# Optimization experiments

Measured on AMD Instinct MI355X. Metric: run time of the kernel, lower is better.

The kernel has to match this reference:

```python
import jax, jax.numpy as jnp
import numpy as np

EMBED_DIM = 1024
NUM_HEADS = 16
HEAD_DIM = EMBED_DIM // NUM_HEADS


def setup_inputs() -> dict:
    key = jax.random.key(0)
    ks = jax.random.split(key, 9)
    B, S, E = 4, 2048, EMBED_DIM
    # xavier_uniform bound for square [E, E] weights
    bound = float(np.sqrt(6.0 / (E + E)))
    def w(k):
        return jax.random.uniform(k, (E, E), jnp.float32, -bound, bound)
    return {
        "x": jax.random.normal(ks[0], (B, S, E), jnp.float32),
        "Wq": w(ks[1]), "bq": jnp.zeros((E,), jnp.float32),
        "Wk": w(ks[2]), "bk": jnp.zeros((E,), jnp.float32),
        "Wv": w(ks[3]), "bv": jnp.zeros((E,), jnp.float32),
        "Wo": w(ks[4]), "bo": jnp.zeros((E,), jnp.float32),
    }


def reference(x, Wq, bq, Wk, bk, Wv, bv, Wo, bo):
    B, S, E = x.shape
    H, D = NUM_HEADS, HEAD_DIM
    # Linear projections (torch Linear: x @ W.T + b)
    q = (x @ Wq.T + bq).reshape(B, S, H, D)
    k = (x @ Wk.T + bk).reshape(B, S, H, D)
    v = (x @ Wv.T + bv).reshape(B, S, H, D)
    # per-head scaled dot-product attention (vectorized over heads)
    scores = jnp.einsum("bqhd,bkhd->bhqk", q, k) / jnp.sqrt(jnp.float32(D))
    attn = jax.nn.softmax(scores, axis=-1)
    o = jnp.einsum("bhqk,bkhd->bqhd", attn, v).reshape(B, S, E)
    return o @ Wo.T + bo
```

## Files before the change

kernel.cpp:

```cpp
#include <hip/hip_runtime.h>
#include <stdint.h>

typedef unsigned short u16;
typedef short bf16x8 __attribute__((ext_vector_type(8)));
typedef float f32x4 __attribute__((ext_vector_type(4)));

#define B_ 4
#define S_ 2048
#define H_ 16
#define D_ 64
#define E_ 1024
#define M_ (B_ * S_)

static __device__ __forceinline__ u16 f2bf(float f) {
  uint32_t u = __builtin_bit_cast(uint32_t, f);
  u += 0x7fffu + ((u >> 16) & 1u);
  return (u16)(u >> 16);
}
static __device__ __forceinline__ u16 hu16(float f) {
  return (u16)((__builtin_bit_cast(uint32_t, f) + 0x8000u) >> 16);
}
static __device__ __forceinline__ uint32_t pack2bf(float a, float b) {
  return (uint32_t)f2bf(a) | ((uint32_t)f2bf(b) << 16);
}

static __device__ __forceinline__ void gld_lds16(const void* g, void* l) {
  __builtin_amdgcn_global_load_lds(
      (const __attribute__((address_space(1))) void*)(uintptr_t)g,
      (__attribute__((address_space(3))) void*)(uint32_t)(uintptr_t)l, 16, 0, 0);
}

template <int ctrl>
static __device__ __forceinline__ float dpp_mov(float x) {
  return __builtin_bit_cast(float,
      __builtin_amdgcn_update_dpp(0, __builtin_bit_cast(int, x), ctrl, 0xF, 0xF, true));
}
static __device__ __forceinline__ float rowsum16(float x) {
  x += dpp_mov<0xB1>(x);
  x += dpp_mov<0x4E>(x);
  x += dpp_mov<0x141>(x);
  x += dpp_mov<0x140>(x);
  return x;
}

__global__ __launch_bounds__(256) void cvt_f32_bf16(const float* __restrict__ in,
                                                    u16* __restrict__ out, int n) {
  int i = (blockIdx.x * 256 + threadIdx.x) * 8;
  if (i + 8 > n) return;
  float4 a = *(const float4*)(in + i);
  float4 b = *(const float4*)(in + i + 4);
  struct __align__(16) U8 { u16 h[8]; } u;
  u.h[0] = f2bf(a.x); u.h[1] = f2bf(a.y); u.h[2] = f2bf(a.z); u.h[3] = f2bf(a.w);
  u.h[4] = f2bf(b.x); u.h[5] = f2bf(b.y); u.h[6] = f2bf(b.z); u.h[7] = f2bf(b.w);
  *(U8*)(out + i) = u;
}

template <int KIND, typename OutT>
static __device__ __forceinline__ void gemm128(const u16* __restrict__ A,
                                               const u16* __restrict__ W,
                                               const float* __restrict__ bias,
                                               OutT* __restrict__ C, int m0, int n0,
                                               float scale, u16* As, u16* Bs) {
  const int tid = threadIdx.x;
  const int wave = tid >> 6, lane = tid & 63;
  const int col16 = lane & 15, quad = lane >> 4;
  const int wm = wave >> 1, wn = wave & 1;

  f32x4 acc[4][4] = {};

  const int r0 = tid >> 3;
  const int sg8 = ((tid & 7) ^ (r0 & 7)) * 8;
  const u16* ga = A + (size_t)(m0 + r0) * E_ + sg8;
  const u16* gb = W + (size_t)(n0 + r0) * E_ + sg8;
  u16* lA = As + wave * 512;
  u16* lB = Bs + wave * 512;

  for (int k0 = 0; k0 < E_; k0 += 64) {
    __syncthreads();
#pragma unroll
    for (int i = 0; i < 4; i++) {
      gld_lds16(ga + (size_t)(i * 32) * E_ + k0, lA + i * 2048);
      gld_lds16(gb + (size_t)(i * 32) * E_ + k0, lB + i * 2048);
    }
    asm volatile("s_waitcnt vmcnt(0)" ::: "memory");
    __syncthreads();

    bf16x8 af[4][2], bw[4][2];
#pragma unroll
    for (int mt = 0; mt < 4; mt++)
#pragma unroll
      for (int ks = 0; ks < 2; ks++)
        af[mt][ks] = *(const bf16x8*)&As[(wm * 64 + mt * 16 + col16) * 64 +
                                         (((ks * 4 + quad) ^ (col16 & 7)) * 8)];
#pragma unroll
    for (int nt = 0; nt < 4; nt++)
#pragma unroll
      for (int ks = 0; ks < 2; ks++)
        bw[nt][ks] = *(const bf16x8*)&Bs[(wn * 64 + nt * 16 + col16) * 64 +
                                         (((ks * 4 + quad) ^ (col16 & 7)) * 8)];
#pragma unroll
    for (int ks = 0; ks < 2; ks++)
#pragma unroll
      for (int a = 0; a < 4; a++)
#pragma unroll
        for (int b = 0; b < 4; b++) {
          if constexpr (KIND == 2)
            acc[a][b] = __builtin_amdgcn_mfma_f32_16x16x32_bf16(af[a][ks], bw[b][ks], acc[a][b], 0, 0, 0);
          else
            acc[a][b] = __builtin_amdgcn_mfma_f32_16x16x32_bf16(bw[a][ks], af[b][ks], acc[a][b], 0, 0, 0);
        }
  }

  if constexpr (KIND == 2) {
#pragma unroll
    for (int a = 0; a < 4; a++) {
      int t = m0 + wm * 64 + a * 16 + quad * 4;
      int bb = t >> 11, s = t & (S_ - 1);
#pragma unroll
      for (int b = 0; b < 4; b++) {
        int oc = n0 + wn * 64 + b * 16 + col16;
        int h = oc >> 6, d = oc & 63;
        float bv = bias[oc];
        uint32_t lo = pack2bf(acc[a][b][0] + bv, acc[a][b][1] + bv);
        uint32_t hi = pack2bf(acc[a][b][2] + bv, acc[a][b][3] + bv);
        uint2 pk = {lo, hi};
        *(uint2*)&C[(((size_t)(bb * H_ + h) * D_ + d) * S_) + s] = pk;
      }
    }
  } else {
#pragma unroll
    for (int b = 0; b < 4; b++) {
      int row = m0 + wm * 64 + b * 16 + col16;
#pragma unroll
      for (int a = 0; a < 4; a++) {
        int nc = n0 + wn * 64 + a * 16 + quad * 4;
        float4 bv = *(const float4*)&bias[nc];
        float v0 = (acc[a][b][0] + bv.x) * scale;
        float v1 = (acc[a][b][1] + bv.y) * scale;
        float v2 = (acc[a][b][2] + bv.z) * scale;
        float v3 = (acc[a][b][3] + bv.w) * scale;
        if constexpr (KIND == 0) {
          uint2 pk = {pack2bf(v0, v1), pack2bf(v2, v3)};
          *(uint2*)&((u16*)C)[(size_t)row * E_ + nc] = pk;
        } else {
          float4 pk = {v0, v1, v2, v3};
          *(float4*)&((float*)C)[(size_t)row * E_ + nc] = pk;
        }
      }
    }
  }
}

__global__ __launch_bounds__(256) void gemm_qkv(const u16* __restrict__ xb,
                                                const u16* __restrict__ wq, const u16* __restrict__ wk,
                                                const u16* __restrict__ wv,
                                                const float* __restrict__ bq, const float* __restrict__ bk,
                                                const float* __restrict__ bv,
                                                u16* __restrict__ Qb, u16* __restrict__ Kb,
                                                u16* __restrict__ Vtb) {
  __shared__ __align__(16) u16 As[128 * 64];
  __shared__ __align__(16) u16 Bs[128 * 64];
  const int mat = blockIdx.x >> 3;
  const int n0 = (blockIdx.x & 7) * 128;
  const int m0 = blockIdx.y * 128;
  if (mat == 0)
    gemm128<0, u16>(xb, wq, bq, Qb, m0, n0, 0.125f * 1.44269504f, As, Bs);
  else if (mat == 1)
    gemm128<0, u16>(xb, wk, bk, Kb, m0, n0, 1.0f, As, Bs);
  else
    gemm128<2, u16>(xb, wv, bv, Vtb, m0, n0, 1.0f, As, Bs);
}

__global__ __launch_bounds__(256) void gemm_out(const u16* __restrict__ Ob,
                                                const u16* __restrict__ wob,
                                                const float* __restrict__ bo,
                                                float* __restrict__ out) {
  __shared__ __align__(16) u16 As[128 * 64];
  __shared__ __align__(16) u16 Bs[128 * 64];
  gemm128<1, float>(Ob, wob, bo, out, blockIdx.y * 128, blockIdx.x * 128, 1.0f, As, Bs);
}

__global__ __launch_bounds__(256) void flash_attn(const u16* __restrict__ Q,
                                                  const u16* __restrict__ K,
                                                  const u16* __restrict__ Vt,
                                                  u16* __restrict__ O) {
  __shared__ __align__(16) u16 Ks[2][64 * 64];
  __shared__ __align__(16) u16 Vs[2][64 * 64];
  __shared__ __align__(16) u16 Ps[4][32 * 72];
  const int bid = blockIdx.x;
  const int qt = bid & 15, h = (bid >> 4) & 15, b = bid >> 8;
  const int tid = threadIdx.x;
  const int wave = tid >> 6, lane = tid & 63;
  const int col16 = lane & 15, quad = lane >> 4;

  bf16x8 qf[2][2];
  const int qrow = qt * 128 + wave * 32;
#pragma unroll
  for (int mt = 0; mt < 2; mt++) {
    const u16* qp = Q + ((size_t)(b * S_ + qrow + mt * 16 + col16) * H_ + h) * D_ + quad * 8;
    qf[mt][0] = *(const bf16x8*)qp;
    qf[mt][1] = *(const bf16x8*)(qp + 32);
  }

  f32x4 o_acc[2][4] = {};
  float l_i[2][4] = {};

  const int srow = tid >> 3;
  const int sgrp = (tid & 7) ^ (srow & 7);
  const u16* Kbase = K + ((size_t)(b * S_) * H_ + h) * D_;
  const u16* Vbase = Vt + ((size_t)(b * H_ + h) * D_) * S_;
  u16* Pw = &Ps[wave][0];

  auto stage = [&](int kb, int buf) {
#pragma unroll
    for (int i = 0; i < 2; i++) {
      gld_lds16(Kbase + (size_t)(kb * 64 + i * 32 + srow) * (H_ * D_) + sgrp * 8,
                &Ks[buf][i * 2048 + wave * 512]);
      gld_lds16(Vbase + (size_t)(i * 32 + srow) * S_ + kb * 64 + sgrp * 8,
                &Vs[buf][i * 2048 + wave * 512]);
    }
  };

  stage(0, 0);
  for (int kb = 0; kb < S_ / 64; kb++) {
    const int cur = kb & 1;
    asm volatile("s_waitcnt vmcnt(0)" ::: "memory");
    __syncthreads();
    if (kb + 1 < S_ / 64) stage(kb + 1, cur ^ 1);
    const u16* KsC = Ks[cur];
    const u16* VsC = Vs[cur];

    f32x4 sacc[2][4] = {};
#pragma unroll
    for (int ks = 0; ks < 2; ks++) {
      bf16x8 kf[4];
#pragma unroll
      for (int nt = 0; nt < 4; nt++)
        kf[nt] = *(const bf16x8*)&KsC[(nt * 16 + col16) * 64 +
                                      (((ks * 4 + quad) ^ (col16 & 7)) * 8)];
#pragma unroll
      for (int mt = 0; mt < 2; mt++)
#pragma unroll
        for (int nt = 0; nt < 4; nt++)
          sacc[mt][nt] = __builtin_amdgcn_mfma_f32_16x16x32_bf16(qf[mt][ks], kf[nt], sacc[mt][nt], 0, 0, 0);
    }

#pragma unroll
    for (int mt = 0; mt < 2; mt++) {
#pragma unroll
      for (int e = 0; e < 4; e++) {
        float p0 = __builtin_amdgcn_exp2f(sacc[mt][0][e]);
        float p1 = __builtin_amdgcn_exp2f(sacc[mt][1][e]);
        float p2 = __builtin_amdgcn_exp2f(sacc[mt][2][e]);
        float p3 = __builtin_amdgcn_exp2f(sacc[mt][3][e]);
        l_i[mt][e] += (p0 + p1) + (p2 + p3);
        const int r = mt * 16 + quad * 4 + e;
        const int ro = r * 72;
        const int cb = col16 + ((r & 8) ? 16 : 0);
        Pw[ro + (cb & 63)] = hu16(p0);
        Pw[ro + ((cb + 16) & 63)] = hu16(p1);
        Pw[ro + ((cb + 32) & 63)] = hu16(p2);
        Pw[ro + ((cb + 48) & 63)] = hu16(p3);
      }
    }
    asm volatile("s_waitcnt lgkmcnt(0)" ::: "memory");

#pragma unroll
    for (int ks = 0; ks < 2; ks++) {
      bf16x8 pf[2], vf[4];
#pragma unroll
      for (int mt = 0; mt < 2; mt++)
        pf[mt] = *(const bf16x8*)&Pw[(mt * 16 + col16) * 72 +
                                     (((ks * 4 + quad + ((col16 >> 3) << 1)) & 7) * 8)];
#pragma unroll
      for (int nt = 0; nt < 4; nt++)
        vf[nt] = *(const bf16x8*)&VsC[(nt * 16 + col16) * 64 +
                                      (((ks * 4 + quad) ^ (col16 & 7)) * 8)];
#pragma unroll
      for (int mt = 0; mt < 2; mt++)
#pragma unroll
        for (int nt = 0; nt < 4; nt++)
          o_acc[mt][nt] = __builtin_amdgcn_mfma_f32_16x16x32_bf16(pf[mt], vf[nt], o_acc[mt][nt], 0, 0, 0);
    }
  }

#pragma unroll
  for (int mt = 0; mt < 2; mt++) {
#pragma unroll
    for (int e = 0; e < 4; e++) {
      float inv = 1.f / rowsum16(l_i[mt][e]);
      int s = qrow + mt * 16 + quad * 4 + e;
#pragma unroll
      for (int nt = 0; nt < 4; nt++)
        O[((size_t)(b * S_ + s) * H_ + h) * D_ + nt * 16 + col16] =
            f2bf(o_acc[mt][nt][e] * inv);
    }
  }
}

extern "C" void kernel_launch(void* const* d_in, const int* in_sizes, int n_in,
                              void* d_out, int out_size, void* d_ws, size_t ws_size,
                              hipStream_t stream) {
  (void)in_sizes; (void)n_in; (void)out_size; (void)ws_size;
  const float* x  = (const float*)d_in[0];
  const float* Wq = (const float*)d_in[1];
  const float* bq = (const float*)d_in[2];
  const float* Wk = (const float*)d_in[3];
  const float* bk = (const float*)d_in[4];
  const float* Wv = (const float*)d_in[5];
  const float* bv = (const float*)d_in[6];
  const float* Wo = (const float*)d_in[7];
  const float* bo = (const float*)d_in[8];
  float* out = (float*)d_out;

  const size_t NX = (size_t)M_ * E_;
  const size_t NW = (size_t)E_ * E_;
  u16* xb  = (u16*)d_ws;
  u16* wqb = xb + NX;
  u16* wkb = wqb + NW;
  u16* wvb = wkb + NW;
  u16* wob = wvb + NW;
  u16* Qb  = wob + NW;
  u16* Kb  = Qb + NX;
  u16* Vtb = Kb + NX;
  u16* Ob  = Vtb + NX;

  cvt_f32_bf16<<<NX / 2048, 256, 0, stream>>>(x, xb, (int)NX);
  cvt_f32_bf16<<<NW / 2048, 256, 0, stream>>>(Wq, wqb, (int)NW);
  cvt_f32_bf16<<<NW / 2048, 256, 0, stream>>>(Wk, wkb, (int)NW);
  cvt_f32_bf16<<<NW / 2048, 256, 0, stream>>>(Wv, wvb, (int)NW);
  cvt_f32_bf16<<<NW / 2048, 256, 0, stream>>>(Wo, wob, (int)NW);

  gemm_qkv<<<dim3(24, 64), 256, 0, stream>>>(xb, wqb, wkb, wvb, bq, bk, bv, Qb, Kb, Vtb);
  flash_attn<<<B_ * H_ * (S_ / 128), 256, 0, stream>>>(Qb, Kb, Vtb, Ob);
  gemm_out<<<dim3(8, 64), 256, 0, stream>>>(Ob, wob, bo, out);
}
```

Measured before the change: 303.2 us.

## Merge conversion launches, reorder attention block mapping, and restage V loads in-loop

Replaces the five f32-to-bf16 conversion launches with one kernel that picks its source by index range, which removes launch overhead. In flash attention, the block index mapping now puts heads and batches in the low bits so that blocks running concurrently share query tiles across heads. V becomes single-buffered and is loaded inside the iteration, with finer vmcnt waits and raw barriers so the V load overlaps the QK^T and softmax phase. This frees LDS, which may raise occupancy, but it relies on careful manual wait counts and redundantly prefetches K on the last iteration.

```diff
diff --git a/kernel.cpp b/kernel.cpp
--- a/kernel.cpp
+++ b/kernel.cpp
@@ -43,16 +43,28 @@
   return x;
 }
 
-__global__ __launch_bounds__(256) void cvt_f32_bf16(const float* __restrict__ in,
-                                                    u16* __restrict__ out, int n) {
+#define NXE (M_ * E_)
+#define NWE (E_ * E_)
+__global__ __launch_bounds__(256) void cvt_all(const float* __restrict__ x,
+                                               const float* __restrict__ Wq,
+                                               const float* __restrict__ Wk,
+                                               const float* __restrict__ Wv,
+                                               const float* __restrict__ Wo,
+                                               u16* __restrict__ ws) {
   int i = (blockIdx.x * 256 + threadIdx.x) * 8;
-  if (i + 8 > n) return;
-  float4 a = *(const float4*)(in + i);
-  float4 b = *(const float4*)(in + i + 4);
+  const float* src;
+  u16* dst = ws + i;
+  if (i < NXE) { src = x + i; }
+  else if (i < NXE + NWE)     { src = Wq + (i - NXE); }
+  else if (i < NXE + 2 * NWE) { src = Wk + (i - NXE - NWE); }
+  else if (i < NXE + 3 * NWE) { src = Wv + (i - NXE - 2 * NWE); }
+  else                        { src = Wo + (i - NXE - 3 * NWE); }
+  float4 a = *(const float4*)src;
+  float4 b = *(const float4*)(src + 4);
   struct __align__(16) U8 { u16 h[8]; } u;
   u.h[0] = f2bf(a.x); u.h[1] = f2bf(a.y); u.h[2] = f2bf(a.z); u.h[3] = f2bf(a.w);
   u.h[4] = f2bf(b.x); u.h[5] = f2bf(b.y); u.h[6] = f2bf(b.z); u.h[7] = f2bf(b.w);
-  *(U8*)(out + i) = u;
+  *(U8*)dst = u;
 }
 
 template <int KIND, typename OutT>
@@ -121,9 +133,8 @@
         int oc = n0 + wn * 64 + b * 16 + col16;
         int h = oc >> 6, d = oc & 63;
         float bv = bias[oc];
-        uint32_t lo = pack2bf(acc[a][b][0] + bv, acc[a][b][1] + bv);
-        uint32_t hi = pack2bf(acc[a][b][2] + bv, acc[a][b][3] + bv);
-        uint2 pk = {lo, hi};
+        uint2 pk = {pack2bf(acc[a][b][0] + bv, acc[a][b][1] + bv),
+                    pack2bf(acc[a][b][2] + bv, acc[a][b][3] + bv)};
         *(uint2*)&C[(((size_t)(bb * H_ + h) * D_ + d) * S_) + s] = pk;
       }
     }
@@ -185,10 +196,10 @@
                                                   const u16* __restrict__ Vt,
                                                   u16* __restrict__ O) {
   __shared__ __align__(16) u16 Ks[2][64 * 64];
-  __shared__ __align__(16) u16 Vs[2][64 * 64];
+  __shared__ __align__(16) u16 Vs[64 * 64];
   __shared__ __align__(16) u16 Ps[4][32 * 72];
   const int bid = blockIdx.x;
-  const int qt = bid & 15, h = (bid >> 4) & 15, b = bid >> 8;
+  const int qt = bid >> 6, h = bid & 15, b = (bid >> 4) & 3;
   const int tid = threadIdx.x;
   const int wave = tid >> 6, lane = tid & 63;
   const int col16 = lane & 15, quad = lane >> 4;
@@ -211,24 +222,28 @@
   const u16* Vbase = Vt + ((size_t)(b * H_ + h) * D_) * S_;
   u16* Pw = &Ps[wave][0];
 
-  auto stage = [&](int kb, int buf) {
-#pragma unroll
-    for (int i = 0; i < 2; i++) {
+  auto stageK = [&](int kb, int buf) {
+#pragma unroll
+    for (int i = 0; i < 2; i++)
       gld_lds16(Kbase + (size_t)(kb * 64 + i * 32 + srow) * (H_ * D_) + sgrp * 8,
                 &Ks[buf][i * 2048 + wave * 512]);
+  };
+  auto stageV = [&](int kb) {
+#pragma unroll
+    for (int i = 0; i < 2; i++)
       gld_lds16(Vbase + (size_t)(i * 32 + srow) * S_ + kb * 64 + sgrp * 8,
-                &Vs[buf][i * 2048 + wave * 512]);
-    }
+                &Vs[i * 2048 + wave * 512]);
   };
 
-  stage(0, 0);
+  stageK(0, 0);
   for (int kb = 0; kb < S_ / 64; kb++) {
     const int cur = kb & 1;
-    asm volatile("s_waitcnt vmcnt(0)" ::: "memory");
-    __syncthreads();
-    if (kb + 1 < S_ / 64) stage(kb + 1, cur ^ 1);
+    asm volatile("s_barrier" ::: "memory");
+    stageV(kb);
+    stageK((kb + 1) & 31, cur ^ 1);
+    asm volatile("s_waitcnt vmcnt(4)" ::: "memory");
+    asm volatile("s_barrier" ::: "memory");
     const u16* KsC = Ks[cur];
-    const u16* VsC = Vs[cur];
 
     f32x4 sacc[2][4] = {};
 #pragma unroll
@@ -264,6 +279,8 @@
       }
     }
     asm volatile("s_waitcnt lgkmcnt(0)" ::: "memory");
+    asm volatile("s_waitcnt vmcnt(2)" ::: "memory");
+    asm volatile("s_barrier" ::: "memory");
 
 #pragma unroll
     for (int ks = 0; ks < 2; ks++) {
@@ -274,8 +291,8 @@
                                      (((ks * 4 + quad + ((col16 >> 3) << 1)) & 7) * 8)];
 #pragma unroll
       for (int nt = 0; nt < 4; nt++)
-        vf[nt] = *(const bf16x8*)&VsC[(nt * 16 + col16) * 64 +
-                                      (((ks * 4 + quad) ^ (col16 & 7)) * 8)];
+        vf[nt] = *(const bf16x8*)&Vs[(nt * 16 + col16) * 64 +
+                                     (((ks * 4 + quad) ^ (col16 & 7)) * 8)];
 #pragma unroll
       for (int mt = 0; mt < 2; mt++)
 #pragma unroll
@@ -325,11 +342,7 @@
   u16* Vtb = Kb + NX;
   u16* Ob  = Vtb + NX;
 
-  cvt_f32_bf16<<<NX / 2048, 256, 0, stream>>>(x, xb, (int)NX);
-  cvt_f32_bf16<<<NW / 2048, 256, 0, stream>>>(Wq, wqb, (int)NW);
-  cvt_f32_bf16<<<NW / 2048, 256, 0, stream>>>(Wk, wkb, (int)NW);
-  cvt_f32_bf16<<<NW / 2048, 256, 0, stream>>>(Wv, wvb, (int)NW);
-  cvt_f32_bf16<<<NW / 2048, 256, 0, stream>>>(Wo, wob, (int)NW);
+  cvt_all<<<(NX + 4 * NW) / 2048, 256, 0, stream>>>(x, Wq, Wk, Wv, Wo, xb);
 
   gemm_qkv<<<dim3(24, 64), 256, 0, stream>>>(xb, wqb, wkb, wvb, bq, bk, bv, Qb, Kb, Vtb);
   flash_attn<<<B_ * H_ * (S_ / 128), 256, 0, stream>>>(Qb, Kb, Vtb, Ob);
```

Measured after the change: 307.1 us. About the same (+1.3%).
